# Kernel tuning notes

Measured on AMD Instinct MI355X. Metric: run time of the kernel, lower is better.

Reference implementation:

```python
import jax, jax.numpy as jnp
import numpy as np

N = 100000       # nodes
E = 3200000      # edges
DIN = 128        # input_dim
H = 64           # hidden_dim
DEMB = 32        # embedding_dim
G = 256          # num graphs


def setup_inputs() -> dict:
    key = jax.random.key(0)
    ks = jax.random.split(key, 10)
    x = jax.random.normal(ks[0], (N, DIN), dtype=jnp.float32)
    edge_index = jax.random.randint(ks[1], (2, E), 0, N, dtype=jnp.int64)
    batch = jnp.sort(jax.random.randint(ks[2], (N,), 0, G, dtype=jnp.int64))
    W1 = jax.random.normal(ks[3], (DIN, H), dtype=jnp.float32) * (1.0 / np.sqrt(DIN))
    b1 = jnp.zeros((H,), dtype=jnp.float32)
    W2 = jax.random.normal(ks[4], (H, H), dtype=jnp.float32) * (1.0 / np.sqrt(H))
    b2 = jnp.zeros((H,), dtype=jnp.float32)
    Wl = jax.random.normal(ks[5], (H, DEMB), dtype=jnp.float32) * (1.0 / np.sqrt(H))
    bl = jnp.zeros((DEMB,), dtype=jnp.float32)
    return {"x": x, "edge_index": edge_index, "batch": batch, "num_graphs": G,
            "W1": W1, "b1": b1, "W2": W2, "b2": b2, "Wl": Wl, "bl": bl}


def _gcn_conv(h, src, dst, W, b, n_nodes):
    # PyG GCNConv: add self-loops, symmetric D^{-1/2}(A+I)D^{-1/2} normalization,
    # linear transform first, then propagate.
    h = h @ W                                                  # [N, out]
    deg = jax.ops.segment_sum(jnp.ones((src.shape[0],), h.dtype), dst,
                              num_segments=n_nodes) + 1.0      # +1 self-loop
    dinv = jax.lax.rsqrt(deg)                                  # [N]
    coef = dinv[src] * dinv[dst]                               # [E]
    msgs = h[src] * coef[:, None]                              # [E, out]
    agg = jax.ops.segment_sum(msgs, dst, num_segments=n_nodes)
    agg = agg + h * (dinv * dinv)[:, None]                     # self-loop message
    return agg + b


def reference(x, edge_index, batch, num_graphs, W1, b1, W2, b2, Wl, bl):
    src, dst = edge_index[0], edge_index[1]
    n_nodes = x.shape[0]
    h = jax.nn.relu(_gcn_conv(x, src, dst, W1, b1, n_nodes))
    h = jax.nn.relu(_gcn_conv(h, src, dst, W2, b2, n_nodes))
    # global_mean_pool over batch ids
    sums = jax.ops.segment_sum(h, batch, num_segments=num_graphs)     # [G, H]
    counts = jax.ops.segment_sum(jnp.ones((n_nodes,), h.dtype), batch,
                                 num_segments=num_graphs)
    pooled = sums / jnp.maximum(counts, 1.0)[:, None]
    return pooled @ Wl + bl                                           # [G, DEMB]
```

## Files before the change

kernel.cpp:

```cpp
#include <hip/hip_runtime.h>

#define NN 100000
#define NE 3200000
#define DIN 128
#define HD 64
#define DEMB 32
#define NG 256
#define NBUCK ((NN + 255) / 256)
#define NPB 512
#define CHUNK ((NE + NPB - 1) / NPB)
#define NM (NBUCK * NPB)
#define NMB ((NM + 1023) / 1024)

typedef unsigned short u16;
typedef unsigned int u32;
typedef __attribute__((ext_vector_type(8))) short bf16x8;
typedef __attribute__((ext_vector_type(4))) float f32x4;

__device__ __forceinline__ float bflo(u32 u) { return __uint_as_float(u << 16); }
__device__ __forceinline__ float bfhi(u32 u) { return __uint_as_float(u & 0xffff0000u); }
__device__ __forceinline__ u16 f2bf(float f) {
    u32 u = __float_as_uint(f);
    return (u16)((u + 0x7fffu + ((u >> 16) & 1u)) >> 16);
}

__global__ __launch_bounds__(256) void k_blkhist(const int* __restrict__ dst,
                                                 int* __restrict__ HM, int E) {
    __shared__ int h[NBUCK];
    int blk = blockIdx.x, t = threadIdx.x;
    for (int i = t; i < NBUCK; i += 256) h[i] = 0;
    __syncthreads();
    int beg = blk * CHUNK, end = min(E, beg + CHUNK);
    for (int j = beg + t; j < end; j += 256) atomicAdd(&h[dst[j] >> 8], 1);
    __syncthreads();
    for (int i = t; i < NBUCK; i += 256) HM[i * NPB + blk] = h[i];
}

__global__ __launch_bounds__(1024) void k_scanA(int* __restrict__ HM,
                                                int* __restrict__ bsum, int n) {
    __shared__ int s[1024];
    int t = threadIdx.x;
    int idx = blockIdx.x * 1024 + t;
    int v = (idx < n) ? HM[idx] : 0;
    s[t] = v;
    __syncthreads();
    for (int off = 1; off < 1024; off <<= 1) {
        int add = (t >= off) ? s[t - off] : 0;
        __syncthreads();
        s[t] += add;
        __syncthreads();
    }
    if (idx < n) HM[idx] = s[t] - v;
    if (t == 1023) bsum[blockIdx.x] = s[t];
}

__global__ __launch_bounds__(256) void k_scan2(const int* __restrict__ bsum,
                                               int* __restrict__ boff, int nb) {
    __shared__ int s[256];
    int t = threadIdx.x;
    int v = (t < nb) ? bsum[t] : 0;
    s[t] = v;
    __syncthreads();
    for (int off = 1; off < 256; off <<= 1) {
        int add = (t >= off) ? s[t - off] : 0;
        __syncthreads();
        s[t] += add;
        __syncthreads();
    }
    if (t < nb) boff[t] = s[t] - v;
    if (t == nb - 1) boff[nb] = s[t];
}

__global__ void k_scanC(int* __restrict__ HM, const int* __restrict__ boff, int n) {
    int idx = blockIdx.x * blockDim.x + threadIdx.x;
    if (idx < n) HM[idx] += boff[idx >> 10];
}

__global__ __launch_bounds__(256) void k_place(const int* __restrict__ src,
                                               const int* __restrict__ dst,
                                               const int* __restrict__ HM,
                                               int* __restrict__ part, int E) {
    __shared__ int cur[NBUCK];
    int blk = blockIdx.x, t = threadIdx.x;
    for (int i = t; i < NBUCK; i += 256) cur[i] = HM[i * NPB + blk];
    __syncthreads();
    int beg = blk * CHUNK, end = min(E, beg + CHUNK);
    for (int j = beg + t; j < end; j += 256) {
        int d = dst[j], s = src[j];
        int pos = atomicAdd(&cur[d >> 8], 1);
        part[pos] = s | ((d & 255) << 17);
    }
}

__global__ __launch_bounds__(256) void k_phaseB(const int* __restrict__ part,
                                                const int* __restrict__ HM,
                                                int* __restrict__ rowptr,
                                                int* __restrict__ ssrc,
                                                float* __restrict__ dinv, int E) {
    __shared__ int cnt[256];
    __shared__ int sc[256];
    int b = blockIdx.x;
    int t = threadIdx.x;
    int beg = HM[b * NPB];
    int end = (b == NBUCK - 1) ? E : HM[(b + 1) * NPB];
    int node0 = b << 8;
    int nnode = NN - node0 < 256 ? NN - node0 : 256;
    cnt[t] = 0;
    __syncthreads();
    for (int j = beg + t; j < end; j += 256) atomicAdd(&cnt[part[j] >> 17], 1);
    __syncthreads();
    int v = cnt[t];
    sc[t] = v;
    __syncthreads();
    for (int off = 1; off < 256; off <<= 1) {
        int add = (t >= off) ? sc[t - off] : 0;
        __syncthreads();
        sc[t] += add;
        __syncthreads();
    }
    int excl = sc[t] - v;
    if (t < nnode) {
        rowptr[node0 + t] = beg + excl;
        dinv[node0 + t] = rsqrtf((float)v + 1.0f);
    }
    if (b == NBUCK - 1 && t == 0) rowptr[NN] = E;
    __syncthreads();
    cnt[t] = beg + excl;
    __syncthreads();
    for (int j = beg + t; j < end; j += 256) {
        int e = part[j];
        int pos = atomicAdd(&cnt[e >> 17], 1);
        ssrc[pos] = e & 0x1FFFF;
    }
}

template <int K, typename XT>
__global__ __launch_bounds__(256, 4) void k_gemm(const XT* __restrict__ X,
                                                 const float* __restrict__ W,
                                                 const float* __restrict__ dinv,
                                                 u16* __restrict__ U, int n) {
    constexpr int XS = K + 8;
    __shared__ __align__(16) u16 xb[64 * XS];
    __shared__ __align__(16) u16 wt[64 * XS];
    int tid = threadIdx.x;
    int lane = tid & 63, wid = tid >> 6;
    int row0 = blockIdx.x * 64;
    for (int idx = tid; idx < 64 * (K / 4); idx += 256) {
        int r = idx / (K / 4), c4 = idx % (K / 4);
        int row = row0 + r;
        ushort4 o = {0, 0, 0, 0};
        if (row < n) {
            if constexpr (sizeof(XT) == 4) {
                float4 v = *reinterpret_cast<const float4*>(&X[(size_t)row * K + c4 * 4]);
                o.x = f2bf(v.x); o.y = f2bf(v.y); o.z = f2bf(v.z); o.w = f2bf(v.w);
            } else {
                o = *reinterpret_cast<const ushort4*>(&X[(size_t)row * K + c4 * 4]);
            }
        }
        *reinterpret_cast<ushort4*>(&xb[r * XS + c4 * 4]) = o;
    }
    for (int idx = tid; idx < K * 64; idx += 256) {
        int k = idx >> 6, c = idx & 63;
        wt[c * XS + k] = f2bf(W[(size_t)k * 64 + c]);
    }
    __syncthreads();
    int lr = lane & 15, kb = lane >> 4;
    f32x4 acc0 = {0.f, 0.f, 0.f, 0.f};
    f32x4 acc1 = {0.f, 0.f, 0.f, 0.f};
    f32x4 acc2 = {0.f, 0.f, 0.f, 0.f};
    f32x4 acc3 = {0.f, 0.f, 0.f, 0.f};
#pragma unroll
    for (int kc = 0; kc < K; kc += 32) {
        bf16x8 a  = *reinterpret_cast<const bf16x8*>(&xb[(wid * 16 + lr) * XS + kc + kb * 8]);
        bf16x8 b0 = *reinterpret_cast<const bf16x8*>(&wt[( 0 + lr) * XS + kc + kb * 8]);
        bf16x8 b1 = *reinterpret_cast<const bf16x8*>(&wt[(16 + lr) * XS + kc + kb * 8]);
        bf16x8 b2 = *reinterpret_cast<const bf16x8*>(&wt[(32 + lr) * XS + kc + kb * 8]);
        bf16x8 b3 = *reinterpret_cast<const bf16x8*>(&wt[(48 + lr) * XS + kc + kb * 8]);
        acc0 = __builtin_amdgcn_mfma_f32_16x16x32_bf16(a, b0, acc0, 0, 0, 0);
        acc1 = __builtin_amdgcn_mfma_f32_16x16x32_bf16(a, b1, acc1, 0, 0, 0);
        acc2 = __builtin_amdgcn_mfma_f32_16x16x32_bf16(a, b2, acc2, 0, 0, 0);
        acc3 = __builtin_amdgcn_mfma_f32_16x16x32_bf16(a, b3, acc3, 0, 0, 0);
    }
#pragma unroll
    for (int reg = 0; reg < 4; ++reg) {
        int row = row0 + wid * 16 + kb * 4 + reg;
        if (row < n) {
            float dv = dinv[row];
            U[(size_t)row * 64 +  0 + lr] = f2bf(acc0[reg] * dv);
            U[(size_t)row * 64 + 16 + lr] = f2bf(acc1[reg] * dv);
            U[(size_t)row * 64 + 32 + lr] = f2bf(acc2[reg] * dv);
            U[(size_t)row * 64 + 48 + lr] = f2bf(acc3[reg] * dv);
        }
    }
}

__global__ void k_gather(const int* __restrict__ rowptr, const int* __restrict__ ssrc,
                         const float* __restrict__ dinv, const u16* __restrict__ U,
                         const float* __restrict__ bias,
                         u16* __restrict__ outbuf, int n) {
    int gtid = blockIdx.x * blockDim.x + threadIdx.x;
    int lane = gtid & 63;
    int g = lane & 7;
    int c = lane >> 3;
    int w = gtid >> 6;
    int nw = (gridDim.x * blockDim.x) >> 6;
    float bv = bias[lane];
    for (int d = w; d < n; d += nw) {
        int beg = rowptr[d], end = rowptr[d + 1];
        float4 aL0 = {0.f,0.f,0.f,0.f}, aH0 = {0.f,0.f,0.f,0.f};
        float4 aL1 = {0.f,0.f,0.f,0.f}, aH1 = {0.f,0.f,0.f,0.f};
        int j = beg;
        for (; j + 16 <= end; j += 16) {
            int s0 = ssrc[j + g];
            int s1 = ssrc[j + 8 + g];
            uint4 u0 = *reinterpret_cast<const uint4*>(&U[(size_t)s0 * 64 + c * 8]);
            uint4 u1 = *reinterpret_cast<const uint4*>(&U[(size_t)s1 * 64 + c * 8]);
            aL0.x += bflo(u0.x); aL0.y += bfhi(u0.x); aL0.z += bflo(u0.y); aL0.w += bfhi(u0.y);
            aH0.x += bflo(u0.z); aH0.y += bfhi(u0.z); aH0.z += bflo(u0.w); aH0.w += bfhi(u0.w);
            aL1.x += bflo(u1.x); aL1.y += bfhi(u1.x); aL1.z += bflo(u1.y); aL1.w += bfhi(u1.y);
            aH1.x += bflo(u1.z); aH1.y += bfhi(u1.z); aH1.z += bflo(u1.w); aH1.w += bfhi(u1.w);
        }
        if (j + 8 <= end) {
            int s0 = ssrc[j + g];
            uint4 u0 = *reinterpret_cast<const uint4*>(&U[(size_t)s0 * 64 + c * 8]);
            aL0.x += bflo(u0.x); aL0.y += bfhi(u0.x); aL0.z += bflo(u0.y); aL0.w += bfhi(u0.y);
            aH0.x += bflo(u0.z); aH0.y += bfhi(u0.z); aH0.z += bflo(u0.w); aH0.w += bfhi(u0.w);
            j += 8;
        }
        if (j + g < end) {
            int s1 = ssrc[j + g];
            uint4 u1 = *reinterpret_cast<const uint4*>(&U[(size_t)s1 * 64 + c * 8]);
            aL1.x += bflo(u1.x); aL1.y += bfhi(u1.x); aL1.z += bflo(u1.y); aL1.w += bfhi(u1.y);
            aH1.x += bflo(u1.z); aH1.y += bfhi(u1.z); aH1.z += bflo(u1.w); aH1.w += bfhi(u1.w);
        }
        aL0.x += aL1.x; aL0.y += aL1.y; aL0.z += aL1.z; aL0.w += aL1.w;
        aH0.x += aH1.x; aH0.y += aH1.y; aH0.z += aH1.z; aH0.w += aH1.w;
#pragma unroll
        for (int m = 1; m <= 4; m <<= 1) {
            aL0.x += __shfl_xor(aL0.x, m); aL0.y += __shfl_xor(aL0.y, m);
            aL0.z += __shfl_xor(aL0.z, m); aL0.w += __shfl_xor(aL0.w, m);
            aH0.x += __shfl_xor(aH0.x, m); aH0.y += __shfl_xor(aH0.y, m);
            aH0.z += __shfl_xor(aH0.z, m); aH0.w += __shfl_xor(aH0.w, m);
        }
        float4 q = (g & 4) ? aH0 : aL0;
        float hv = (g & 2) ? ((g & 1) ? q.w : q.z) : ((g & 1) ? q.y : q.x);
        float ud = __uint_as_float(((u32)U[(size_t)d * 64 + lane]) << 16);
        float dd = dinv[d];
        float h = (hv + ud) * dd + bv;
        h = h > 0.f ? h : 0.f;
        outbuf[(size_t)d * 64 + lane] = f2bf(h);
    }
}

__global__ __launch_bounds__(256) void k_pool(const u16* __restrict__ h,
                                              const int* __restrict__ batch,
                                              float* __restrict__ sums, int n) {
    int tid = blockIdx.x * blockDim.x + threadIdx.x;
    int wave = tid >> 6;
    int lane = tid & 63;
    int node0 = wave * 64;
    if (node0 >= n) return;
    int nodeEnd = min(n, node0 + 64);
    float acc = 0.f;
    int curg = batch[node0];
    for (int nd = node0; nd < nodeEnd; ++nd) {
        int g = batch[nd];
        if (g != curg) {
            atomicAdd(&sums[(size_t)curg * 64 + lane], acc);
            acc = 0.f;
            curg = g;
        }
        acc += __uint_as_float(((u32)h[(size_t)nd * 64 + lane]) << 16);
    }
    atomicAdd(&sums[(size_t)curg * 64 + lane], acc);
}

__global__ void k_final(const float* __restrict__ sums, const int* __restrict__ batch,
                        const float* __restrict__ Wl, const float* __restrict__ bl,
                        float* __restrict__ out, int n) {
    __shared__ float pooled[64];
    int g = blockIdx.x;
    int t = threadIdx.x;
    int lo = 0, hi = n;
    while (lo < hi) { int m = (lo + hi) >> 1; if (batch[m] < g) lo = m + 1; else hi = m; }
    int lo2 = lo, hi2 = n;
    while (lo2 < hi2) { int m = (lo2 + hi2) >> 1; if (batch[m] < g + 1) lo2 = m + 1; else hi2 = m; }
    float c = (float)(lo2 - lo);
    c = c < 1.0f ? 1.0f : c;
    pooled[t] = sums[g * 64 + t] / c;
    __syncthreads();
    if (t < 32) {
        float acc = bl[t];
#pragma unroll 8
        for (int k = 0; k < 64; k++) acc += pooled[k] * Wl[k * 32 + t];
        out[g * 32 + t] = acc;
    }
}

extern "C" void kernel_launch(void* const* d_in, const int* in_sizes, int n_in,
                              void* d_out, int out_size, void* d_ws, size_t ws_size,
                              hipStream_t stream) {
    const float* x = (const float*)d_in[0];
    const int* ei = (const int*)d_in[1];
    const int* batch = (const int*)d_in[2];
    const float* W1 = (const float*)d_in[4];
    const float* b1 = (const float*)d_in[5];
    const float* W2 = (const float*)d_in[6];
    const float* b2 = (const float*)d_in[7];
    const float* Wl = (const float*)d_in[8];
    const float* bl = (const float*)d_in[9];
    float* out = (float*)d_out;

    const int* esrc = ei;
    const int* edst = ei + NE;

    char* ws = (char*)d_ws;
    size_t off = 0;
    auto alloc = [&](size_t bytes) {
        void* p = ws + off;
        off += (bytes + 255) & ~size_t(255);
        return p;
    };
    float* dinv   = (float*)alloc((size_t)NN * 4);
    int*   rowptr = (int*)alloc((size_t)(NN + 1) * 4);
    int*   HM     = (int*)alloc((size_t)NM * 4);
    int*   bsum   = (int*)alloc((size_t)(NMB + 1) * 4);
    int*   boff   = (int*)alloc((size_t)(NMB + 1) * 4);
    int*   ssrc   = (int*)alloc((size_t)NE * 4);
    u16*   tbuf   = (u16*)alloc((size_t)NE * 4);
    u16*   agg    = (u16*)alloc((size_t)NN * HD * 2);
    float* sums   = (float*)alloc((size_t)NG * HD * 4);
    int* part = (int*)tbuf;

    k_blkhist<<<NPB, 256, 0, stream>>>(edst, HM, NE);
    k_scanA<<<NMB, 1024, 0, stream>>>(HM, bsum, NM);
    k_scan2<<<1, 256, 0, stream>>>(bsum, boff, NMB);
    k_scanC<<<(NM + 255) / 256, 256, 0, stream>>>(HM, boff, NM);
    k_place<<<NPB, 256, 0, stream>>>(esrc, edst, HM, part, NE);
    k_phaseB<<<NBUCK, 256, 0, stream>>>(part, HM, rowptr, ssrc, dinv, NE);

    k_gemm<DIN, float><<<(NN + 63) / 64, 256, 0, stream>>>(x, W1, dinv, tbuf, NN);
    k_gather<<<2048, 256, 0, stream>>>(rowptr, ssrc, dinv, tbuf, b1, agg, NN);

    k_gemm<HD, u16><<<(NN + 63) / 64, 256, 0, stream>>>(agg, W2, dinv, tbuf, NN);
    k_gather<<<2048, 256, 0, stream>>>(rowptr, ssrc, dinv, tbuf, b2, agg, NN);

    hipMemsetAsync(sums, 0, (size_t)NG * HD * 4, stream);
    k_pool<<<(NN + 255) / 256, 256, 0, stream>>>(agg, batch, sums, NN);
    k_final<<<NG, 64, 0, stream>>>(sums, batch, Wl, bl, out, NN);
}
```

Baseline: 264.5 us.

## Fold scan fixup into placement kernel and stage bucket edges in LDS

Removes the two small scan kernels (second-level scan and offset add) by having every placement block redo the tiny block-sum scan and add the offsets on the fly. Block 0 also writes compact per-bucket offsets for the next phase. The phaseB kernel now copies each bucket's edges into a 40KB shared buffer when they fit, so the two passes over the bucket read shared memory rather than global memory. This saves two launches and some global traffic, at the cost of redundant scans in each of 512 blocks and extra LDS that may lower occupancy.

```diff
diff --git a/kernel.cpp b/kernel.cpp
--- a/kernel.cpp
+++ b/kernel.cpp
@@ -11,6 +11,7 @@
 #define CHUNK ((NE + NPB - 1) / NPB)
 #define NM (NBUCK * NPB)
 #define NMB ((NM + 1023) / 1024)
+#define BCAP 10240
 
 typedef unsigned short u16;
 typedef unsigned int u32;
@@ -54,35 +55,34 @@
     if (t == 1023) bsum[blockIdx.x] = s[t];
 }
 
-__global__ __launch_bounds__(256) void k_scan2(const int* __restrict__ bsum,
-                                               int* __restrict__ boff, int nb) {
-    __shared__ int s[256];
-    int t = threadIdx.x;
-    int v = (t < nb) ? bsum[t] : 0;
-    s[t] = v;
-    __syncthreads();
-    for (int off = 1; off < 256; off <<= 1) {
-        int add = (t >= off) ? s[t - off] : 0;
-        __syncthreads();
-        s[t] += add;
-        __syncthreads();
-    }
-    if (t < nb) boff[t] = s[t] - v;
-    if (t == nb - 1) boff[nb] = s[t];
-}
-
-__global__ void k_scanC(int* __restrict__ HM, const int* __restrict__ boff, int n) {
-    int idx = blockIdx.x * blockDim.x + threadIdx.x;
-    if (idx < n) HM[idx] += boff[idx >> 10];
-}
-
 __global__ __launch_bounds__(256) void k_place(const int* __restrict__ src,
                                                const int* __restrict__ dst,
                                                const int* __restrict__ HM,
-                                               int* __restrict__ part, int E) {
+                                               const int* __restrict__ bsum,
+                                               int* __restrict__ part,
+                                               int* __restrict__ crow, int E) {
     __shared__ int cur[NBUCK];
+    __shared__ int sb[256];
+    __shared__ int sbe[256];
     int blk = blockIdx.x, t = threadIdx.x;
-    for (int i = t; i < NBUCK; i += 256) cur[i] = HM[i * NPB + blk];
+    int v = (t < NMB) ? bsum[t] : 0;
+    sb[t] = v;
+    __syncthreads();
+    for (int off = 1; off < 256; off <<= 1) {
+        int add = (t >= off) ? sb[t - off] : 0;
+        __syncthreads();
+        sb[t] += add;
+        __syncthreads();
+    }
+    sbe[t] = sb[t] - v;
+    __syncthreads();
+    for (int i = t; i < NBUCK; i += 256) {
+        int idx = i * NPB + blk;
+        int absv = HM[idx] + sbe[idx >> 10];
+        cur[i] = absv;
+        if (blk == 0) crow[i] = absv;
+    }
+    if (blk == 0 && t == 0) crow[NBUCK] = E;
     __syncthreads();
     int beg = blk * CHUNK, end = min(E, beg + CHUNK);
     for (int j = beg + t; j < end; j += 256) {
@@ -93,21 +93,25 @@
 }
 
 __global__ __launch_bounds__(256) void k_phaseB(const int* __restrict__ part,
-                                                const int* __restrict__ HM,
+                                                const int* __restrict__ crow,
                                                 int* __restrict__ rowptr,
                                                 int* __restrict__ ssrc,
                                                 float* __restrict__ dinv, int E) {
     __shared__ int cnt[256];
     __shared__ int sc[256];
+    __shared__ int ebuf[BCAP];
     int b = blockIdx.x;
     int t = threadIdx.x;
-    int beg = HM[b * NPB];
-    int end = (b == NBUCK - 1) ? E : HM[(b + 1) * NPB];
+    int beg = crow[b], end = crow[b + 1];
+    int m = end - beg;
+    bool inLds = (m <= BCAP);
+    if (inLds) for (int j = t; j < m; j += 256) ebuf[j] = part[beg + j];
     int node0 = b << 8;
     int nnode = NN - node0 < 256 ? NN - node0 : 256;
     cnt[t] = 0;
     __syncthreads();
-    for (int j = beg + t; j < end; j += 256) atomicAdd(&cnt[part[j] >> 17], 1);
+    for (int j = t; j < m; j += 256)
+        atomicAdd(&cnt[(inLds ? ebuf[j] : part[beg + j]) >> 17], 1);
     __syncthreads();
     int v = cnt[t];
     sc[t] = v;
@@ -127,8 +131,8 @@
     __syncthreads();
     cnt[t] = beg + excl;
     __syncthreads();
-    for (int j = beg + t; j < end; j += 256) {
-        int e = part[j];
+    for (int j = t; j < m; j += 256) {
+        int e = inLds ? ebuf[j] : part[beg + j];
         int pos = atomicAdd(&cnt[e >> 17], 1);
         ssrc[pos] = e & 0x1FFFF;
     }
@@ -194,6 +198,10 @@
     }
 }
 
+#define ACC8(u, L, H) \
+    L.x += bflo(u.x); L.y += bfhi(u.x); L.z += bflo(u.y); L.w += bfhi(u.y); \
+    H.x += bflo(u.z); H.y += bfhi(u.z); H.z += bflo(u.w); H.w += bfhi(u.w);
+
 __global__ void k_gather(const int* __restrict__ rowptr, const int* __restrict__ ssrc,
                          const float* __restrict__ dinv, const u16* __restrict__ U,
                          const float* __restrict__ bias,
@@ -215,23 +223,18 @@
             int s1 = ssrc[j + 8 + g];
             uint4 u0 = *reinterpret_cast<const uint4*>(&U[(size_t)s0 * 64 + c * 8]);
             uint4 u1 = *reinterpret_cast<const uint4*>(&U[(size_t)s1 * 64 + c * 8]);
-            aL0.x += bflo(u0.x); aL0.y += bfhi(u0.x); aL0.z += bflo(u0.y); aL0.w += bfhi(u0.y);
-            aH0.x += bflo(u0.z); aH0.y += bfhi(u0.z); aH0.z += bflo(u0.w); aH0.w += bfhi(u0.w);
-            aL1.x += bflo(u1.x); aL1.y += bfhi(u1.x); aL1.z += bflo(u1.y); aL1.w += bfhi(u1.y);
-            aH1.x += bflo(u1.z); aH1.y += bfhi(u1.z); aH1.z += bflo(u1.w); aH1.w += bfhi(u1.w);
+            ACC8(u0, aL0, aH0); ACC8(u1, aL1, aH1);
         }
         if (j + 8 <= end) {
             int s0 = ssrc[j + g];
             uint4 u0 = *reinterpret_cast<const uint4*>(&U[(size_t)s0 * 64 + c * 8]);
-            aL0.x += bflo(u0.x); aL0.y += bfhi(u0.x); aL0.z += bflo(u0.y); aL0.w += bfhi(u0.y);
-            aH0.x += bflo(u0.z); aH0.y += bfhi(u0.z); aH0.z += bflo(u0.w); aH0.w += bfhi(u0.w);
+            ACC8(u0, aL0, aH0);
             j += 8;
         }
         if (j + g < end) {
             int s1 = ssrc[j + g];
             uint4 u1 = *reinterpret_cast<const uint4*>(&U[(size_t)s1 * 64 + c * 8]);
-            aL1.x += bflo(u1.x); aL1.y += bfhi(u1.x); aL1.z += bflo(u1.y); aL1.w += bfhi(u1.y);
-            aH1.x += bflo(u1.z); aH1.y += bfhi(u1.z); aH1.z += bflo(u1.w); aH1.w += bfhi(u1.w);
+            ACC8(u1, aL1, aH1);
         }
         aL0.x += aL1.x; aL0.y += aL1.y; aL0.z += aL1.z; aL0.w += aL1.w;
         aH0.x += aH1.x; aH0.y += aH1.y; aH0.z += aH1.z; aH0.w += aH1.w;
@@ -325,7 +328,7 @@
     int*   rowptr = (int*)alloc((size_t)(NN + 1) * 4);
     int*   HM     = (int*)alloc((size_t)NM * 4);
     int*   bsum   = (int*)alloc((size_t)(NMB + 1) * 4);
-    int*   boff   = (int*)alloc((size_t)(NMB + 1) * 4);
+    int*   crow   = (int*)alloc((size_t)(NBUCK + 1) * 4);
     int*   ssrc   = (int*)alloc((size_t)NE * 4);
     u16*   tbuf   = (u16*)alloc((size_t)NE * 4);
     u16*   agg    = (u16*)alloc((size_t)NN * HD * 2);
@@ -334,10 +337,8 @@
 
     k_blkhist<<<NPB, 256, 0, stream>>>(edst, HM, NE);
     k_scanA<<<NMB, 1024, 0, stream>>>(HM, bsum, NM);
-    k_scan2<<<1, 256, 0, stream>>>(bsum, boff, NMB);
-    k_scanC<<<(NM + 255) / 256, 256, 0, stream>>>(HM, boff, NM);
-    k_place<<<NPB, 256, 0, stream>>>(esrc, edst, HM, part, NE);
-    k_phaseB<<<NBUCK, 256, 0, stream>>>(part, HM, rowptr, ssrc, dinv, NE);
+    k_place<<<NPB, 256, 0, stream>>>(esrc, edst, HM, bsum, part, crow, NE);
+    k_phaseB<<<NBUCK, 256, 0, stream>>>(part, crow, rowptr, ssrc, dinv, NE);
 
     k_gemm<DIN, float><<<(NN + 63) / 64, 256, 0, stream>>>(x, W1, dinv, tbuf, NN);
     k_gather<<<2048, 256, 0, stream>>>(rowptr, ssrc, dinv, tbuf, b1, agg, NN);
```

Result: faster. 256.6 us (-3.0%).
